# Performance work log

Hardware: AMD Instinct MI355X
Metric: run time of the kernel (lower is better)

## Reference

```python
import jax, jax.numpy as jnp
import numpy as np

B, T, D, NF = 16, 128, 64, 32
TS, H = 64, 128  # transf_size, lstm hidden


def _lstm_cell(x, h_prev, c_prev, Wih, Whh, bih, bhh):
    # PyTorch gate order: i, f, g, o
    g = x @ Wih.T + h_prev @ Whh.T + bih + bhh
    i, f, gg, o = jnp.split(g, 4, axis=-1)
    c = jax.nn.sigmoid(f) * c_prev + jax.nn.sigmoid(i) * jnp.tanh(gg)
    h = jax.nn.sigmoid(o) * jnp.tanh(c)
    return h, c


def setup_inputs() -> dict:
    key = jax.random.key(0)
    ks = jax.random.split(key, 12)
    s = 1.0 / np.sqrt(H)
    u = lambda k, shape, b=s: jax.random.uniform(k, shape, jnp.float32, -b, b)
    return {
        "X": jax.random.normal(ks[0], (B, T, D, NF), jnp.float32),
        "W_t": u(ks[1], (TS, NF), 1.0 / np.sqrt(NF)),
        "b_t": u(ks[2], (TS,), 1.0 / np.sqrt(NF)),
        "Wih_f": u(ks[3], (4 * H, TS)),
        "Whh_f": u(ks[4], (4 * H, H)),
        "bih_f": u(ks[5], (4 * H,)),
        "bhh_f": u(ks[6], (4 * H,)),
        "Wih_b": u(ks[7], (4 * H, TS)),
        "Whh_b": u(ks[8], (4 * H, H)),
        "bih_b": u(ks[9], (4 * H,)),
        "bhh_b": u(ks[10], (4 * H,)),
        "diag_w": jax.random.uniform(ks[11], (2 * D * H,), jnp.float32, -np.sqrt(5.0), np.sqrt(5.0)),
        "diag_b": jax.random.uniform(jax.random.fold_in(key, 99), (2 * D * H,), jnp.float32, -1.0 / np.sqrt(5.0), 1.0 / np.sqrt(5.0)),
    }


def reference(X, W_t, b_t, Wih_f, Whh_f, bih_f, bhh_f,
              Wih_b, Whh_b, bih_b, bhh_b, diag_w, diag_b):
    b, t_len, d, nf = X.shape
    h = Whh_f.shape[1]
    # feature transform + tanh: [b,T,d,ts]
    out = jnp.tanh(X @ W_t.T + b_t)
    # [b,d,T,ts] -> [b*d, T, ts]
    out = jnp.swapaxes(out, 1, 2).reshape(b * d, t_len, -1)
    Bp = b * d
    xs = jnp.swapaxes(out, 0, 1)  # [T, Bp, ts]

    # Because the original code feeds the bidirectional LSTM one timestep at a
    # time while carrying (h, c), BOTH directions act as forward recurrences.
    def step(carry, x):
        hf, cf, hb, cb = carry
        hf, cf = _lstm_cell(x, hf, cf, Wih_f, Whh_f, bih_f, bhh_f)
        hb, cb = _lstm_cell(x, hb, cb, Wih_b, Whh_b, bih_b, bhh_b)
        return (hf, cf, hb, cb), jnp.concatenate([hf, hb], axis=-1)

    z = jnp.zeros((Bp, h), X.dtype)
    _, hvec = jax.lax.scan(step, (z, z, z, z), xs)  # [T, Bp, 2h]
    hvec = jnp.swapaxes(hvec, 0, 1)  # [Bp, T, 2h]

    # attention pooling against last hidden state
    hT = hvec[:, -1, :]  # [Bp, 2h]
    wgts = jax.nn.softmax(jnp.einsum('bth,bh->bt', hvec, hT), axis=1)
    pooled = jnp.einsum('bth,bt->bh', hvec, wgts)  # [Bp, 2h]

    # context normalization across the d*2h per-sample vector
    X2 = pooled.reshape(b, d * 2 * h)
    m = jnp.mean(X2, axis=1, keepdims=True)
    s = jnp.std(X2, axis=1, keepdims=True, ddof=1)  # torch.std is unbiased
    outn = (X2 - m) / s * diag_w + diag_b
    return outn.reshape(b, d, 2 * h)
```

## Files before the change

### kernel.cpp

```cpp
#include <hip/hip_runtime.h>
#include <hip/hip_bf16.h>

#define B_  16
#define T_  128
#define D_  64
#define NF_ 32
#define TS_ 64
#define H_  128

using bf16x8 = __attribute__((ext_vector_type(8))) short;
using f32x4  = __attribute__((ext_vector_type(4))) float;

__device__ __forceinline__ unsigned short f2bf(float x) {
    union { float f; unsigned int u; } v; v.f = x;
    unsigned int u = v.u;
    unsigned int r = (u + 0x7fffu + ((u >> 16) & 1u)) >> 16;
    return (unsigned short)r;
}
__device__ __forceinline__ float rcpf(float x) { return __builtin_amdgcn_rcpf(x); }
__device__ __forceinline__ float sigm(float x) {
    return rcpf(1.0f + __expf(-x));
}
__device__ __forceinline__ float tanhfast(float x) {
    float e = __expf(-2.0f * fabsf(x));
    float t = (1.0f - e) * rcpf(1.0f + e);
    return copysignf(t, x);
}

__global__ __launch_bounds__(256) void k_proj(const float* __restrict__ X,
                                              const float* __restrict__ Wt,
                                              const float* __restrict__ bt,
                                              unsigned short* __restrict__ xs)
{
    __shared__ float sW[TS_ * NF_];
    __shared__ float sb[TS_];
    __shared__ float sX[16 * NF_];
    int g = blockIdx.x, t = blockIdx.y, tid = threadIdx.x;

    for (int i = tid; i < TS_ * NF_; i += 256) sW[i] = Wt[i];
    if (tid < TS_) sb[tid] = bt[tid];
    for (int i = tid; i < 16 * NF_; i += 256) {
        int r = i >> 5, nf = i & 31;
        int bp = g * 16 + r, b = bp >> 6, d = bp & 63;
        sX[i] = X[(((size_t)b * T_ + t) * D_ + d) * NF_ + nf];
    }
    __syncthreads();

    size_t tile = ((size_t)(g * T_ + t)) * 1024;
    for (int idx = tid; idx < 1024; idx += 256) {
        int r = idx >> 6, ts = idx & 63;
        float s = sb[ts];
        const float* w  = &sW[ts * NF_];
        const float* xr = &sX[r * NF_];
        #pragma unroll
        for (int nf = 0; nf < NF_; ++nf) s += xr[nf] * w[nf];
        float v = tanhfast(s);
        int off = ((ts >> 5) << 9) + (((ts & 31) >> 3) << 7) + (r << 3) + (ts & 7);
        xs[tile + off] = f2bf(v);
    }
}

__global__ __launch_bounds__(512, 2) void k_lstm(
    const unsigned short* __restrict__ xs,
    const float* __restrict__ WihF, const float* __restrict__ WhhF,
    const float* __restrict__ bihF, const float* __restrict__ bhhF,
    const float* __restrict__ WihB, const float* __restrict__ WhhB,
    const float* __restrict__ bihB, const float* __restrict__ bhhB,
    float* __restrict__ hvec)
{
    __shared__ __align__(16) unsigned short hl[2][2048];

    int g = blockIdx.x & 63, dir = blockIdx.x >> 6;
    int tid = threadIdx.x, wid = tid >> 6, lane = tid & 63;
    int lhi = lane >> 4, llo = lane & 15;

    const float* Wih = dir ? WihB : WihF;
    const float* Whh = dir ? WhhB : WhhF;
    const float* bih = dir ? bihB : bihF;
    const float* bhh = dir ? bhhB : bhhF;

    int jb = wid << 4;
    bf16x8 whh[4][4], wih[4][2];
    float bias[4];
    #pragma unroll
    for (int gt = 0; gt < 4; ++gt) {
        int n = gt * H_ + jb + llo;
        bias[gt] = bih[n] + bhh[n];
        const float* wr = Whh + (size_t)n * H_;
        #pragma unroll
        for (int kt = 0; kt < 4; ++kt) {
            const float* p = wr + kt * 32 + lhi * 8;
            bf16x8 v;
            #pragma unroll
            for (int e = 0; e < 8; ++e) v[e] = (short)f2bf(p[e]);
            whh[gt][kt] = v;
        }
        const float* wr2 = Wih + (size_t)n * TS_;
        #pragma unroll
        for (int kt = 0; kt < 2; ++kt) {
            const float* p = wr2 + kt * 32 + lhi * 8;
            bf16x8 v;
            #pragma unroll
            for (int e = 0; e < 8; ++e) v[e] = (short)f2bf(p[e]);
            wih[gt][kt] = v;
        }
    }

    for (int i = tid; i < 1024; i += 512) ((unsigned int*)hl[0])[i] = 0u;

    float c[4] = {0.f, 0.f, 0.f, 0.f};
    int j = jb + llo;
    int jelem = ((j >> 5) << 9) + (((j & 31) >> 3) << 7) + (j & 7);
    int r0 = lhi * 4;
    const unsigned short* xsg = xs + ((size_t)g * T_) * 1024;

    asm volatile("s_waitcnt lgkmcnt(0)" ::: "memory");
    __builtin_amdgcn_s_barrier();
    __builtin_amdgcn_sched_barrier(0);

    bf16x8 nx0 = *(const bf16x8*)(xsg + lane * 8);
    bf16x8 nx1 = *(const bf16x8*)(xsg + 512 + lane * 8);

    int cur = 0;
    for (int t = 0; t < T_; ++t) {
        bf16x8 ax0 = nx0, ax1 = nx1;
        int tn = (t < T_ - 1) ? t + 1 : t;
        nx0 = *(const bf16x8*)(xsg + (size_t)tn * 1024 + lane * 8);
        nx1 = *(const bf16x8*)(xsg + (size_t)tn * 1024 + 512 + lane * 8);

        bf16x8 ah[4];
        #pragma unroll
        for (int kt = 0; kt < 4; ++kt)
            ah[kt] = *(const bf16x8*)(hl[cur] + kt * 512 + lane * 8);

        f32x4 acc[4];
        #pragma unroll
        for (int gt = 0; gt < 4; ++gt) {
            f32x4 a = {bias[gt], bias[gt], bias[gt], bias[gt]};
            a = __builtin_amdgcn_mfma_f32_16x16x32_bf16(ax0, wih[gt][0], a, 0, 0, 0);
            a = __builtin_amdgcn_mfma_f32_16x16x32_bf16(ax1, wih[gt][1], a, 0, 0, 0);
            #pragma unroll
            for (int kt = 0; kt < 4; ++kt)
                a = __builtin_amdgcn_mfma_f32_16x16x32_bf16(ah[kt], whh[gt][kt], a, 0, 0, 0);
            acc[gt] = a;
        }

        float hv[4];
        #pragma unroll
        for (int s = 0; s < 4; ++s) {
            float iv = sigm(acc[0][s]);
            float fv = sigm(acc[1][s]);
            float gv = tanhfast(acc[2][s]);
            float ov = sigm(acc[3][s]);
            float cn = fv * c[s] + iv * gv;
            c[s] = cn;
            hv[s] = ov * tanhfast(cn);
        }

        int nxt = cur ^ 1;
        #pragma unroll
        for (int s = 0; s < 4; ++s) hl[nxt][jelem + (r0 + s) * 8] = f2bf(hv[s]);

        #pragma unroll
        for (int s = 0; s < 4; ++s) {
            int bp = g * 16 + r0 + s;
            hvec[((size_t)bp * T_ + t) * 256 + dir * H_ + j] = hv[s];
        }

        asm volatile("s_waitcnt lgkmcnt(0)" ::: "memory");
        __builtin_amdgcn_s_barrier();
        __builtin_amdgcn_sched_barrier(0);
        cur = nxt;
    }
}

__global__ __launch_bounds__(256, 1) void k_attn(const float* __restrict__ hvec,
                                                 float* __restrict__ pooled)
{
    __shared__ float sh[T_ * 256];
    __shared__ float sc[T_];
    int bp = blockIdx.x, tid = threadIdx.x;

    const float4* src = (const float4*)(hvec + (size_t)bp * T_ * 256);
    float4* dst = (float4*)sh;
    #pragma unroll
    for (int i = 0; i < 32; ++i) dst[tid + i * 256] = src[tid + i * 256];
    __syncthreads();

    int wid = tid >> 6, lane = tid & 63;
    float4 q = *(const float4*)&sh[127 * 256 + lane * 4];
    #pragma unroll 4
    for (int r = 0; r < 32; ++r) {
        int t = wid + r * 4;
        float4 hr = *(const float4*)&sh[t * 256 + lane * 4];
        float s = hr.x * q.x + hr.y * q.y + hr.z * q.z + hr.w * q.w;
        s += __shfl_xor(s, 32); s += __shfl_xor(s, 16); s += __shfl_xor(s, 8);
        s += __shfl_xor(s, 4);  s += __shfl_xor(s, 2);  s += __shfl_xor(s, 1);
        if (lane == 0) sc[t] = s;
    }
    __syncthreads();

    float m = -1e30f;
    for (int t2 = 0; t2 < T_; ++t2) m = fmaxf(m, sc[t2]);
    __syncthreads();
    if (tid < T_) sc[tid] = __expf(sc[tid] - m);
    __syncthreads();
    float ssum = 0.f;
    for (int t2 = 0; t2 < T_; ++t2) ssum += sc[t2];
    float inv = 1.0f / ssum;

    float a = 0.f;
    #pragma unroll 8
    for (int t2 = 0; t2 < T_; ++t2) a += sc[t2] * sh[t2 * 256 + tid];
    pooled[(size_t)bp * 256 + tid] = a * inv;
}

__global__ __launch_bounds__(256) void k_norm(const float* __restrict__ pooled,
                                              const float* __restrict__ dw,
                                              const float* __restrict__ db,
                                              float* __restrict__ out)
{
    __shared__ double rs[256], rq[256];
    int b = blockIdx.x, tid = threadIdx.x;
    const float* xp = pooled + (size_t)b * 16384;
    double s = 0.0, q = 0.0;
    for (int i = tid; i < 16384; i += 256) { double x = xp[i]; s += x; q += x * x; }
    rs[tid] = s; rq[tid] = q;
    __syncthreads();
    for (int o = 128; o > 0; o >>= 1) {
        if (tid < o) { rs[tid] += rs[tid + o]; rq[tid] += rq[tid + o]; }
        __syncthreads();
    }
    double N = 16384.0;
    double mean = rs[0] / N;
    double var = (rq[0] - N * mean * mean) / (N - 1.0);
    float m = (float)mean;
    float invs = (float)(1.0 / sqrt(var));
    for (int i = tid; i < 16384; i += 256) {
        float x = xp[i];
        out[(size_t)b * 16384 + i] = (x - m) * invs * dw[i] + db[i];
    }
}

extern "C" void kernel_launch(void* const* d_in, const int* in_sizes, int n_in,
                              void* d_out, int out_size, void* d_ws, size_t ws_size,
                              hipStream_t stream)
{
    const float* X    = (const float*)d_in[0];
    const float* Wt   = (const float*)d_in[1];
    const float* bt   = (const float*)d_in[2];
    const float* WihF = (const float*)d_in[3];
    const float* WhhF = (const float*)d_in[4];
    const float* bihF = (const float*)d_in[5];
    const float* bhhF = (const float*)d_in[6];
    const float* WihB = (const float*)d_in[7];
    const float* WhhB = (const float*)d_in[8];
    const float* bihB = (const float*)d_in[9];
    const float* bhhB = (const float*)d_in[10];
    const float* dw   = (const float*)d_in[11];
    const float* db   = (const float*)d_in[12];
    float* out = (float*)d_out;

    char* ws = (char*)d_ws;
    unsigned short* xs = (unsigned short*)(ws);
    float* hvec   = (float*)(ws + 16777216);
    float* pooled = (float*)(ws + 16777216 + 134217728);

    k_proj<<<dim3(64, 128), 256, 0, stream>>>(X, Wt, bt, xs);
    k_lstm<<<128, 512, 0, stream>>>(xs, WihF, WhhF, bihF, bhhF,
                                        WihB, WhhB, bihB, bhhB, hvec);
    k_attn<<<1024, 256, 0, stream>>>(hvec, pooled);
    k_norm<<<16, 256, 0, stream>>>(pooled, dw, db, out);
}
```

Before: 333.8 us.

## Store LSTM hidden states as bf16 and split MFMA accumulation chains

The intermediate hvec buffer changes from fp32 to bf16, halving the LSTM kernel's global writes and the attention kernel's reads and shared-memory footprint, and allowing k_attn to run more than one block per CU. The serial MFMA chain per gate is split into three independent accumulators to shorten the dependency latency on the recurrent critical path. k_proj transposes its weight tile in shared memory with padding to avoid bank conflicts. Attention scores and pooling now use bf16-rounded hidden states, which reduces accuracy.

```diff
diff --git a/kernel.cpp b/kernel.cpp
--- a/kernel.cpp
+++ b/kernel.cpp
@@ -9,6 +9,7 @@
 #define H_  128
 
 using bf16x8 = __attribute__((ext_vector_type(8))) short;
+using bf16x4 = __attribute__((ext_vector_type(4))) short;
 using f32x4  = __attribute__((ext_vector_type(4))) float;
 
 __device__ __forceinline__ unsigned short f2bf(float x) {
@@ -17,6 +18,10 @@
     unsigned int r = (u + 0x7fffu + ((u >> 16) & 1u)) >> 16;
     return (unsigned short)r;
 }
+__device__ __forceinline__ float bf2f(unsigned short u) {
+    union { unsigned int u; float f; } v; v.u = ((unsigned int)u) << 16;
+    return v.f;
+}
 __device__ __forceinline__ float rcpf(float x) { return __builtin_amdgcn_rcpf(x); }
 __device__ __forceinline__ float sigm(float x) {
     return rcpf(1.0f + __expf(-x));
@@ -32,12 +37,15 @@
                                               const float* __restrict__ bt,
                                               unsigned short* __restrict__ xs)
 {
-    __shared__ float sW[TS_ * NF_];
+    __shared__ float sWt[NF_ * 65];
     __shared__ float sb[TS_];
     __shared__ float sX[16 * NF_];
     int g = blockIdx.x, t = blockIdx.y, tid = threadIdx.x;
 
-    for (int i = tid; i < TS_ * NF_; i += 256) sW[i] = Wt[i];
+    for (int i = tid; i < TS_ * NF_; i += 256) {
+        int ts = i >> 5, nf = i & 31;
+        sWt[nf * 65 + ts] = Wt[i];
+    }
     if (tid < TS_) sb[tid] = bt[tid];
     for (int i = tid; i < 16 * NF_; i += 256) {
         int r = i >> 5, nf = i & 31;
@@ -50,10 +58,9 @@
     for (int idx = tid; idx < 1024; idx += 256) {
         int r = idx >> 6, ts = idx & 63;
         float s = sb[ts];
-        const float* w  = &sW[ts * NF_];
         const float* xr = &sX[r * NF_];
         #pragma unroll
-        for (int nf = 0; nf < NF_; ++nf) s += xr[nf] * w[nf];
+        for (int nf = 0; nf < NF_; ++nf) s += xr[nf] * sWt[nf * 65 + ts];
         float v = tanhfast(s);
         int off = ((ts >> 5) << 9) + (((ts & 31) >> 3) << 7) + (r << 3) + (ts & 7);
         xs[tile + off] = f2bf(v);
@@ -66,7 +73,7 @@
     const float* __restrict__ bihF, const float* __restrict__ bhhF,
     const float* __restrict__ WihB, const float* __restrict__ WhhB,
     const float* __restrict__ bihB, const float* __restrict__ bhhB,
-    float* __restrict__ hvec)
+    unsigned short* __restrict__ hvec)
 {
     __shared__ __align__(16) unsigned short hl[2][2048];
 
@@ -113,6 +120,7 @@
     int jelem = ((j >> 5) << 9) + (((j & 31) >> 3) << 7) + (j & 7);
     int r0 = lhi * 4;
     const unsigned short* xsg = xs + ((size_t)g * T_) * 1024;
+    size_t rowoff = ((size_t)(g * 16 + r0) * T_) * 256 + dir * H_ + j;
 
     asm volatile("s_waitcnt lgkmcnt(0)" ::: "memory");
     __builtin_amdgcn_s_barrier();
@@ -136,13 +144,16 @@
         f32x4 acc[4];
         #pragma unroll
         for (int gt = 0; gt < 4; ++gt) {
-            f32x4 a = {bias[gt], bias[gt], bias[gt], bias[gt]};
-            a = __builtin_amdgcn_mfma_f32_16x16x32_bf16(ax0, wih[gt][0], a, 0, 0, 0);
-            a = __builtin_amdgcn_mfma_f32_16x16x32_bf16(ax1, wih[gt][1], a, 0, 0, 0);
-            #pragma unroll
-            for (int kt = 0; kt < 4; ++kt)
-                a = __builtin_amdgcn_mfma_f32_16x16x32_bf16(ah[kt], whh[gt][kt], a, 0, 0, 0);
-            acc[gt] = a;
+            f32x4 aX = {bias[gt], bias[gt], bias[gt], bias[gt]};
+            aX = __builtin_amdgcn_mfma_f32_16x16x32_bf16(ax0, wih[gt][0], aX, 0, 0, 0);
+            aX = __builtin_amdgcn_mfma_f32_16x16x32_bf16(ax1, wih[gt][1], aX, 0, 0, 0);
+            f32x4 aH1 = {0.f, 0.f, 0.f, 0.f};
+            aH1 = __builtin_amdgcn_mfma_f32_16x16x32_bf16(ah[0], whh[gt][0], aH1, 0, 0, 0);
+            aH1 = __builtin_amdgcn_mfma_f32_16x16x32_bf16(ah[1], whh[gt][1], aH1, 0, 0, 0);
+            f32x4 aH2 = {0.f, 0.f, 0.f, 0.f};
+            aH2 = __builtin_amdgcn_mfma_f32_16x16x32_bf16(ah[2], whh[gt][2], aH2, 0, 0, 0);
+            aH2 = __builtin_amdgcn_mfma_f32_16x16x32_bf16(ah[3], whh[gt][3], aH2, 0, 0, 0);
+            acc[gt] = aX + aH1 + aH2;
         }
 
         float hv[4];
@@ -158,14 +169,16 @@
         }
 
         int nxt = cur ^ 1;
-        #pragma unroll
-        for (int s = 0; s < 4; ++s) hl[nxt][jelem + (r0 + s) * 8] = f2bf(hv[s]);
-
-        #pragma unroll
-        for (int s = 0; s < 4; ++s) {
-            int bp = g * 16 + r0 + s;
-            hvec[((size_t)bp * T_ + t) * 256 + dir * H_ + j] = hv[s];
-        }
+        unsigned short hb[4];
+        #pragma unroll
+        for (int s = 0; s < 4; ++s) hb[s] = f2bf(hv[s]);
+        #pragma unroll
+        for (int s = 0; s < 4; ++s) hl[nxt][jelem + (r0 + s) * 8] = hb[s];
+
+        #pragma unroll
+        for (int s = 0; s < 4; ++s)
+            hvec[rowoff + (size_t)s * (T_ * 256)] = hb[s];
+        rowoff += 256;
 
         asm volatile("s_waitcnt lgkmcnt(0)" ::: "memory");
         __builtin_amdgcn_s_barrier();
@@ -174,26 +187,29 @@
     }
 }
 
-__global__ __launch_bounds__(256, 1) void k_attn(const float* __restrict__ hvec,
-                                                 float* __restrict__ pooled)
-{
-    __shared__ float sh[T_ * 256];
+__global__ __launch_bounds__(256) void k_attn(const unsigned short* __restrict__ hvec,
+                                              float* __restrict__ pooled)
+{
+    __shared__ unsigned short sh[T_ * 256];
     __shared__ float sc[T_];
     int bp = blockIdx.x, tid = threadIdx.x;
 
-    const float4* src = (const float4*)(hvec + (size_t)bp * T_ * 256);
-    float4* dst = (float4*)sh;
+    const bf16x8* src = (const bf16x8*)(hvec + (size_t)bp * T_ * 256);
+    bf16x8* dst = (bf16x8*)sh;
     #pragma unroll
-    for (int i = 0; i < 32; ++i) dst[tid + i * 256] = src[tid + i * 256];
+    for (int i = 0; i < 16; ++i) dst[tid + i * 256] = src[tid + i * 256];
     __syncthreads();
 
     int wid = tid >> 6, lane = tid & 63;
-    float4 q = *(const float4*)&sh[127 * 256 + lane * 4];
+    bf16x4 q4 = *(const bf16x4*)&sh[127 * 256 + lane * 4];
+    float q0 = bf2f((unsigned short)q4[0]), q1 = bf2f((unsigned short)q4[1]);
+    float q2 = bf2f((unsigned short)q4[2]), q3 = bf2f((unsigned short)q4[3]);
     #pragma unroll 4
     for (int r = 0; r < 32; ++r) {
         int t = wid + r * 4;
-        float4 hr = *(const float4*)&sh[t * 256 + lane * 4];
-        float s = hr.x * q.x + hr.y * q.y + hr.z * q.z + hr.w * q.w;
+        bf16x4 h4 = *(const bf16x4*)&sh[t * 256 + lane * 4];
+        float s = bf2f((unsigned short)h4[0]) * q0 + bf2f((unsigned short)h4[1]) * q1
+                + bf2f((unsigned short)h4[2]) * q2 + bf2f((unsigned short)h4[3]) * q3;
         s += __shfl_xor(s, 32); s += __shfl_xor(s, 16); s += __shfl_xor(s, 8);
         s += __shfl_xor(s, 4);  s += __shfl_xor(s, 2);  s += __shfl_xor(s, 1);
         if (lane == 0) sc[t] = s;
@@ -211,7 +227,7 @@
 
     float a = 0.f;
     #pragma unroll 8
-    for (int t2 = 0; t2 < T_; ++t2) a += sc[t2] * sh[t2 * 256 + tid];
+    for (int t2 = 0; t2 < T_; ++t2) a += sc[t2] * bf2f(sh[t2 * 256 + tid]);
     pooled[(size_t)bp * 256 + tid] = a * inv;
 }
 
@@ -262,9 +278,9 @@
     float* out = (float*)d_out;
 
     char* ws = (char*)d_ws;
-    unsigned short* xs = (unsigned short*)(ws);
-    float* hvec   = (float*)(ws + 16777216);
-    float* pooled = (float*)(ws + 16777216 + 134217728);
+    unsigned short* xs   = (unsigned short*)(ws);
+    unsigned short* hvec = (unsigned short*)(ws + (16u << 20));
+    float* pooled        = (float*)(ws + (16u << 20) + (64u << 20));
 
     k_proj<<<dim3(64, 128), 256, 0, stream>>>(X, Wt, bt, xs);
     k_lstm<<<128, 512, 0, stream>>>(xs, WihF, WhhF, bihF, bhhF,
```

Result: faster. 321.9 us (-3.6%).
